# Kernel tuning notes

Hardware: AMD Instinct MI355X
Metric: run time of the kernel (lower is better)

The kernel has to match this reference:

```python
import jax, jax.numpy as jnp
import numpy as np

B, S, D, H = 4, 2048, 1024, 16
DK = D // H

def setup_inputs() -> dict:
    key = jax.random.key(0)
    ks = jax.random.split(key, 8)
    scale = 1.0 / np.sqrt(D)
    return {
        'q': jax.random.normal(ks[0], (B, S, D), jnp.float32),
        'k': jax.random.normal(ks[1], (B, S, D), jnp.float32),
        'v': jax.random.normal(ks[2], (B, S, D), jnp.float32),
        'Wq': jax.random.normal(ks[3], (D, D), jnp.float32) * scale,
        'bq': jnp.zeros((D,), jnp.float32),
        'Wk': jax.random.normal(ks[4], (D, D), jnp.float32) * scale,
        'bk': jnp.zeros((D,), jnp.float32),
        'Wv': jax.random.normal(ks[5], (D, D), jnp.float32) * scale,
        'bv': jnp.zeros((D,), jnp.float32),
        'Wo': jax.random.normal(ks[6], (D, D), jnp.float32) * scale,
        'bo': jnp.zeros((D,), jnp.float32),
    }

def reference(q, k, v, Wq, bq, Wk, bk, Wv, bv, Wo, bo):
    # Linear projections (torch Linear: x @ W.T + b; here W stored as [in,out])
    qp = q @ Wq + bq  # [B,S,D]
    kp = k @ Wk + bk
    vp = v @ Wv + bv
    # split heads -> [B,H,S,DK]
    qh = qp.reshape(B, S, H, DK).transpose(0, 2, 1, 3)
    kh = kp.reshape(B, S, H, DK).transpose(0, 2, 1, 3)
    vh = vp.reshape(B, S, H, DK).transpose(0, 2, 1, 3)
    scores = jnp.einsum('bhqd,bhkd->bhqk', qh, kh) / jnp.sqrt(jnp.float32(DK))
    attn = jax.nn.softmax(scores, axis=-1)  # [B,H,S,S]
    out = jnp.einsum('bhqk,bhkd->bhqd', attn, vh)
    out = out.transpose(0, 2, 1, 3).reshape(B, S, D)
    return out @ Wo + bo
```

## Files before the change

### kernel.cpp

```cpp
#include <hip/hip_runtime.h>
#include <math.h>

#define SEQ 2048
#define DIM 1024
#define NH 16

typedef short s8v __attribute__((ext_vector_type(8)));
typedef float f4v __attribute__((ext_vector_type(4)));

__device__ __forceinline__ unsigned short f2bf(float x) {
    unsigned u = __float_as_uint(x);
    u += 0x7FFFu + ((u >> 16) & 1u);
    return (unsigned short)(u >> 16);
}
__device__ __forceinline__ unsigned cvt_pk_bf16(float lo, float hi) {
    unsigned r;
    asm("v_cvt_pk_bf16_f32 %0, %1, %2" : "=v"(r) : "v"(lo), "v"(hi));
    return r;
}

__global__ void conv3_f32_bf16(const float* __restrict__ q, const float* __restrict__ k,
                               const float* __restrict__ v,
                               unsigned short* __restrict__ qb, unsigned short* __restrict__ kb,
                               unsigned short* __restrict__ vb, int n4) {
    const float* in = (blockIdx.y == 0) ? q : (blockIdx.y == 1) ? k : v;
    unsigned short* out = (blockIdx.y == 0) ? qb : (blockIdx.y == 1) ? kb : vb;
    int i = blockIdx.x * 256 + threadIdx.x;
    if (i >= n4) return;
    float4 x = ((const float4*)in)[i];
    ushort4 o;
    o.x = f2bf(x.x); o.y = f2bf(x.y); o.z = f2bf(x.z); o.w = f2bf(x.w);
    ((ushort4*)out)[i] = o;
}

__global__ __launch_bounds__(256)
void convT4_f32_bf16(const float* __restrict__ W0, const float* __restrict__ W1,
                     const float* __restrict__ W2, const float* __restrict__ W3,
                     unsigned short* __restrict__ T0, unsigned short* __restrict__ T1,
                     unsigned short* __restrict__ T2, unsigned short* __restrict__ T3) {
    const float* W = (blockIdx.z == 0) ? W0 : (blockIdx.z == 1) ? W1 : (blockIdx.z == 2) ? W2 : W3;
    unsigned short* WT = (blockIdx.z == 0) ? T0 : (blockIdx.z == 1) ? T1 : (blockIdx.z == 2) ? T2 : T3;
    __shared__ float T[64][65];
    const int t = threadIdx.x;
    const int n0 = blockIdx.x * 64, k0 = blockIdx.y * 64;
    #pragma unroll
    for (int i = 0; i < 4; i++) {
        int idx = t + i * 256;
        int r = idx >> 4, c4 = idx & 15;
        float4 v = *(const float4*)&W[(size_t)(k0 + r) * DIM + n0 + c4 * 4];
        T[r][c4 * 4 + 0] = v.x; T[r][c4 * 4 + 1] = v.y;
        T[r][c4 * 4 + 2] = v.z; T[r][c4 * 4 + 3] = v.w;
    }
    __syncthreads();
    #pragma unroll
    for (int i = 0; i < 4; i++) {
        int idx = t + i * 256;
        int rn = idx >> 4, c4 = idx & 15;
        ushort4 o;
        o.x = f2bf(T[c4 * 4 + 0][rn]);
        o.y = f2bf(T[c4 * 4 + 1][rn]);
        o.z = f2bf(T[c4 * 4 + 2][rn]);
        o.w = f2bf(T[c4 * 4 + 3][rn]);
        *(ushort4*)&WT[(size_t)(n0 + rn) * DIM + k0 + c4 * 4] = o;
    }
}

template<int MODE>
__device__ __forceinline__
void gemm_core(const unsigned short* __restrict__ A,
               const unsigned short* __restrict__ BT,
               const float* __restrict__ bias, void* __restrict__ outp,
               float scale, int bx, int by)
{
    __shared__ __align__(16) unsigned short As[128 * 64];
    __shared__ __align__(16) unsigned short Bs[128 * 64];
    const int t = threadIdx.x;
    const int lane = t & 63, w = t >> 6;
    const int l15 = lane & 15, quad = lane >> 4;
    const int bm = by * 128, bn = bx * 128;
    const int wm = (w & 1) * 64, wn = (w >> 1) * 64;
    const int lrow = lane >> 3, lcol = (lane & 7) * 8;

    f4v acc[4][4];
    #pragma unroll
    for (int mi = 0; mi < 4; mi++)
        #pragma unroll
        for (int ni = 0; ni < 4; ni++)
            acc[mi][ni] = (f4v){0.f, 0.f, 0.f, 0.f};

    for (int k0 = 0; k0 < DIM; k0 += 64) {
        __syncthreads();
        #pragma unroll
        for (int i = 0; i < 4; i++) {
            int ci = w + i * 4;
            int row = ci * 8 + lrow;
            __builtin_amdgcn_global_load_lds(
                (const __attribute__((address_space(1))) unsigned int*)
                    (A + (size_t)(bm + row) * DIM + k0 + lcol),
                (__attribute__((address_space(3))) unsigned int*)(As + ci * 8 * 64),
                16, 0, 0);
            __builtin_amdgcn_global_load_lds(
                (const __attribute__((address_space(1))) unsigned int*)
                    (BT + (size_t)(bn + row) * DIM + k0 + lcol),
                (__attribute__((address_space(3))) unsigned int*)(Bs + ci * 8 * 64),
                16, 0, 0);
        }
        __syncthreads();
        #pragma unroll
        for (int kc = 0; kc < 2; kc++) {
            const int ko = kc * 32 + quad * 8;
            s8v af[4], bf[4];
            #pragma unroll
            for (int mi = 0; mi < 4; mi++)
                af[mi] = *(const s8v*)&As[(wm + mi * 16 + l15) * 64 + ko];
            #pragma unroll
            for (int ni = 0; ni < 4; ni++)
                bf[ni] = *(const s8v*)&Bs[(wn + ni * 16 + l15) * 64 + ko];
            #pragma unroll
            for (int mi = 0; mi < 4; mi++)
                #pragma unroll
                for (int ni = 0; ni < 4; ni++)
                    acc[mi][ni] = __builtin_amdgcn_mfma_f32_16x16x32_bf16(
                        af[mi], bf[ni], acc[mi][ni], 0, 0, 0);
        }
    }

    #pragma unroll
    for (int mi = 0; mi < 4; mi++) {
        #pragma unroll
        for (int ni = 0; ni < 4; ni++) {
            #pragma unroll
            for (int r = 0; r < 4; r++) {
                int m = bm + wm + mi * 16 + quad * 4 + r;
                int n = bn + wn + ni * 16 + l15;
                float val = acc[mi][ni][r] + bias[n];
                if (MODE == 0) {
                    ((float*)outp)[(size_t)m * DIM + n] = val;
                } else {
                    val *= scale;
                    int b = m >> 11, s = m & (SEQ - 1);
                    int h = n >> 6, dk = n & 63;
                    ((unsigned short*)outp)[(((size_t)(b * NH + h)) * SEQ + s) * 64 + dk] = f2bf(val);
                }
            }
        }
    }
}

__global__ __launch_bounds__(256)
void qkv_gemm(const unsigned short* __restrict__ qb, const unsigned short* __restrict__ kb,
              const unsigned short* __restrict__ vb,
              const unsigned short* __restrict__ WqT, const unsigned short* __restrict__ WkT,
              const unsigned short* __restrict__ WvT,
              const float* __restrict__ bq, const float* __restrict__ bk,
              const float* __restrict__ bv,
              unsigned short* __restrict__ qp, unsigned short* __restrict__ kp,
              unsigned short* __restrict__ vp)
{
    const int z = blockIdx.z;
    const unsigned short* A  = (z == 0) ? qb : (z == 1) ? kb : vb;
    const unsigned short* BT = (z == 0) ? WqT : (z == 1) ? WkT : WvT;
    const float* bias        = (z == 0) ? bq : (z == 1) ? bk : bv;
    unsigned short* outp     = (z == 0) ? qp : (z == 1) ? kp : vp;
    float scale = (z == 0) ? 0.18033688011112042f : 1.0f;
    gemm_core<1>(A, BT, bias, outp, scale, blockIdx.x, blockIdx.y);
}

__global__ __launch_bounds__(256)
void out_gemm(const unsigned short* __restrict__ A, const unsigned short* __restrict__ BT,
              const float* __restrict__ bias, float* __restrict__ outp)
{
    gemm_core<0>(A, BT, bias, outp, 1.0f, blockIdx.x, blockIdx.y);
}

__global__ __launch_bounds__(256)
void transp_v(const unsigned short* __restrict__ vp, unsigned short* __restrict__ vpT) {
    __shared__ unsigned short T[64 * 72];
    const int t = threadIdx.x;
    const int bh = blockIdx.y, s0 = blockIdx.x * 64;
    const int r = t >> 3, c = (t & 7) * 8;
    #pragma unroll
    for (int i = 0; i < 2; i++) {
        int row = r + i * 32;
        *(s8v*)&T[row * 72 + c] = *(const s8v*)&vp[((size_t)bh * SEQ + s0 + row) * 64 + c];
    }
    __syncthreads();
    #pragma unroll
    for (int i = 0; i < 2; i++) {
        int d = r + i * 32;
        s8v o;
        #pragma unroll
        for (int j = 0; j < 8; j++) o[j] = (short)T[(c + j) * 72 + d];
        *(s8v*)&vpT[((size_t)bh * 64 + d) * SEQ + s0 + c] = o;
    }
}

__global__ __launch_bounds__(256)
void attn_mfma(const unsigned short* __restrict__ Q,
               const unsigned short* __restrict__ Kp,
               const unsigned short* __restrict__ VT,
               unsigned short* __restrict__ AO)
{
    __shared__ __align__(16) unsigned short Ks[64 * 72];
    __shared__ __align__(16) unsigned short Vs[64 * 72];
    __shared__ __align__(16) unsigned short Ps[4][32 * 72];
    const int t = threadIdx.x;
    const int lane = t & 63, w = t >> 6;
    const int l15 = lane & 15, quad = lane >> 4;
    const int bh = blockIdx.y, q0 = blockIdx.x * 128;

    const unsigned short* qbase = Q + ((size_t)bh * SEQ + q0 + w * 32) * 64;
    const unsigned short* kbase = Kp + (size_t)bh * SEQ * 64;
    const unsigned short* vtbase = VT + (size_t)bh * 64 * SEQ;

    s8v qf[2][2];
    #pragma unroll
    for (int qs = 0; qs < 2; qs++)
        #pragma unroll
        for (int kc = 0; kc < 2; kc++)
            qf[qs][kc] = *(const s8v*)&qbase[(qs * 16 + l15) * 64 + kc * 32 + quad * 8];

    f4v o_acc[2][4];
    #pragma unroll
    for (int qs = 0; qs < 2; qs++)
        #pragma unroll
        for (int df = 0; df < 4; df++) o_acc[qs][df] = (f4v){0.f, 0.f, 0.f, 0.f};
    float l_part[2] = {0.f, 0.f};

    const int srow = t >> 3, scol = (t & 7) * 8;
    unsigned short* Pw = (unsigned short*)Ps[w];

    s8v kreg[2], vreg[2];
    #pragma unroll
    for (int i = 0; i < 2; i++) {
        int row = srow + i * 32;
        kreg[i] = *(const s8v*)&kbase[(size_t)row * 64 + scol];
        vreg[i] = *(const s8v*)&vtbase[(size_t)row * SEQ + scol];
    }
    #pragma unroll
    for (int i = 0; i < 2; i++) {
        int row = srow + i * 32;
        *(s8v*)&Ks[row * 72 + scol] = kreg[i];
        *(s8v*)&Vs[row * 72 + scol] = vreg[i];
    }
    __syncthreads();

    for (int kt = 0; kt < 32; kt++) {
        if (kt < 31) {
            #pragma unroll
            for (int i = 0; i < 2; i++) {
                int row = srow + i * 32;
                kreg[i] = *(const s8v*)&kbase[((size_t)((kt + 1) * 64 + row)) * 64 + scol];
                vreg[i] = *(const s8v*)&vtbase[(size_t)row * SEQ + (kt + 1) * 64 + scol];
            }
        }

        f4v s_acc[2][4];
        #pragma unroll
        for (int qs = 0; qs < 2; qs++)
            #pragma unroll
            for (int mf = 0; mf < 4; mf++) s_acc[qs][mf] = (f4v){0.f, 0.f, 0.f, 0.f};
        __builtin_amdgcn_s_setprio(1);
        #pragma unroll
        for (int kc = 0; kc < 2; kc++) {
            const int ko = kc * 32 + quad * 8;
            #pragma unroll
            for (int mf = 0; mf < 4; mf++) {
                s8v kf = *(const s8v*)&Ks[(mf * 16 + l15) * 72 + ko];
                #pragma unroll
                for (int qs = 0; qs < 2; qs++)
                    s_acc[qs][mf] = __builtin_amdgcn_mfma_f32_16x16x32_bf16(
                        kf, qf[qs][kc], s_acc[qs][mf], 0, 0, 0);
            }
        }
        __builtin_amdgcn_s_setprio(0);

        #pragma unroll
        for (int qs = 0; qs < 2; qs++) {
            #pragma unroll
            for (int mf = 0; mf < 4; mf++) {
                float p0 = __builtin_amdgcn_exp2f(s_acc[qs][mf][0]);
                float p1 = __builtin_amdgcn_exp2f(s_acc[qs][mf][1]);
                float p2 = __builtin_amdgcn_exp2f(s_acc[qs][mf][2]);
                float p3 = __builtin_amdgcn_exp2f(s_acc[qs][mf][3]);
                l_part[qs] += (p0 + p1) + (p2 + p3);
                uint2 pk;
                pk.x = cvt_pk_bf16(p0, p1);
                pk.y = cvt_pk_bf16(p2, p3);
                *(uint2*)&Pw[(qs * 16 + l15) * 72 + mf * 16 + quad * 4] = pk;
            }
        }

        #pragma unroll
        for (int kc2 = 0; kc2 < 2; kc2++) {
            const int ko = kc2 * 32 + quad * 8;
            s8v pf0 = *(const s8v*)&Pw[(0 * 16 + l15) * 72 + ko];
            s8v pf1 = *(const s8v*)&Pw[(1 * 16 + l15) * 72 + ko];
            __builtin_amdgcn_s_setprio(1);
            #pragma unroll
            for (int df = 0; df < 4; df++) {
                s8v vf = *(const s8v*)&Vs[(df * 16 + l15) * 72 + ko];
                o_acc[0][df] = __builtin_amdgcn_mfma_f32_16x16x32_bf16(pf0, vf, o_acc[0][df], 0, 0, 0);
                o_acc[1][df] = __builtin_amdgcn_mfma_f32_16x16x32_bf16(pf1, vf, o_acc[1][df], 0, 0, 0);
            }
            __builtin_amdgcn_s_setprio(0);
        }

        __syncthreads();
        if (kt < 31) {
            #pragma unroll
            for (int i = 0; i < 2; i++) {
                int row = srow + i * 32;
                *(s8v*)&Ks[row * 72 + scol] = kreg[i];
                *(s8v*)&Vs[row * 72 + scol] = vreg[i];
            }
        }
        __syncthreads();
    }

    float lq[2][4];
    #pragma unroll
    for (int qs = 0; qs < 2; qs++) {
        float lt = l_part[qs];
        lt += __shfl_xor(lt, 16);
        lt += __shfl_xor(lt, 32);
        #pragma unroll
        for (int r = 0; r < 4; r++)
            lq[qs][r] = 1.0f / __shfl(lt, quad * 4 + r);
    }

    const int b = bh >> 4, h = bh & (NH - 1);
    #pragma unroll
    for (int qs = 0; qs < 2; qs++) {
        #pragma unroll
        for (int r = 0; r < 4; r++) {
            int s = q0 + w * 32 + qs * 16 + quad * 4 + r;
            #pragma unroll
            for (int df = 0; df < 4; df++)
                AO[((size_t)(b * SEQ + s)) * DIM + h * 64 + df * 16 + l15] =
                    f2bf(o_acc[qs][df][r] * lq[qs][r]);
        }
    }
}

extern "C" void kernel_launch(void* const* d_in, const int* in_sizes, int n_in,
                              void* d_out, int out_size, void* d_ws, size_t ws_size,
                              hipStream_t stream) {
    const float* q  = (const float*)d_in[0];
    const float* k  = (const float*)d_in[1];
    const float* v  = (const float*)d_in[2];
    const float* Wq = (const float*)d_in[3];
    const float* bq = (const float*)d_in[4];
    const float* Wk = (const float*)d_in[5];
    const float* bk = (const float*)d_in[6];
    const float* Wv = (const float*)d_in[7];
    const float* bv = (const float*)d_in[8];
    const float* Wo = (const float*)d_in[9];
    const float* bo = (const float*)d_in[10];
    float* out = (float*)d_out;

    const size_t MK = (size_t)4 * SEQ * DIM;
    const size_t WK = (size_t)DIM * DIM;
    unsigned short* wsu = (unsigned short*)d_ws;
    unsigned short* qb  = wsu;
    unsigned short* kb  = qb + MK;
    unsigned short* vb  = kb + MK;
    unsigned short* WqT = vb + MK;
    unsigned short* WkT = WqT + WK;
    unsigned short* WvT = WkT + WK;
    unsigned short* WoT = WvT + WK;
    unsigned short* qp  = WoT + WK;
    unsigned short* kp  = qp + MK;
    unsigned short* vp  = kp + MK;
    unsigned short* ao  = vp + MK;
    unsigned short* vpT = qb;

    const int n4 = (int)(MK / 4);
    conv3_f32_bf16<<<dim3((n4 + 255) / 256, 3), 256, 0, stream>>>(q, k, v, qb, kb, vb, n4);
    convT4_f32_bf16<<<dim3(16, 16, 4), 256, 0, stream>>>(Wq, Wk, Wv, Wo, WqT, WkT, WvT, WoT);

    qkv_gemm<<<dim3(DIM / 128, (4 * SEQ) / 128, 3), 256, 0, stream>>>(
        qb, kb, vb, WqT, WkT, WvT, bq, bk, bv, qp, kp, vp);

    transp_v<<<dim3(SEQ / 64, 4 * NH), 256, 0, stream>>>(vp, vpT);

    attn_mfma<<<dim3(SEQ / 128, 4 * NH), 256, 0, stream>>>(qp, kp, vpT, ao);

    out_gemm<<<dim3(DIM / 128, (4 * SEQ) / 128), 256, 0, stream>>>(ao, WoT, bo, out);
}
```

Measured before the change: 379.1 us.

## Fuse V transpose into QKV GEMM epilogue, MFMA row sums, polynomial exp2

The V projection GEMM now writes its output directly in the transposed [bh, d, s] layout through a new epilogue mode, so the separate transpose kernel and its extra memory pass are gone. The attention kernel computes the softmax denominator with an extra MFMA against a ones vector instead of scalar adds and cross-lane shuffles. It also replaces the hardware exp2 with a software polynomial plus ldexp. The polynomial costs more VALU instructions than the native exp2 and may slow the softmax stage. The transposed epilogue writes 4-element strided stores, which may coalesce less well than the old layout.

```diff
diff --git a/kernel.cpp b/kernel.cpp
--- a/kernel.cpp
+++ b/kernel.cpp
@@ -17,6 +17,16 @@
     unsigned r;
     asm("v_cvt_pk_bf16_f32 %0, %1, %2" : "=v"(r) : "v"(lo), "v"(hi));
     return r;
+}
+__device__ __forceinline__ float fast_exp2(float x) {
+    float r = __builtin_rintf(x);
+    float f = x - r;
+    int   e = (int)r;
+    float p = fmaf(f, 0.0096181291f, 0.0555041087f);
+    p = fmaf(f, p, 0.2402265069f);
+    p = fmaf(f, p, 0.6931471806f);
+    p = fmaf(f, p, 1.0f);
+    return ldexpf(p, e);
 }
 
 __global__ void conv3_f32_bf16(const float* __restrict__ q, const float* __restrict__ k,
@@ -129,18 +139,34 @@
     for (int mi = 0; mi < 4; mi++) {
         #pragma unroll
         for (int ni = 0; ni < 4; ni++) {
-            #pragma unroll
-            for (int r = 0; r < 4; r++) {
-                int m = bm + wm + mi * 16 + quad * 4 + r;
+            if (MODE == 2) {
+                ushort4 o;
+                #pragma unroll
+                for (int r = 0; r < 4; r++) {
+                    int m = bm + wm + mi * 16 + quad * 4 + r;
+                    int n = bn + wn + ni * 16 + l15;
+                    float val = acc[mi][ni][r] + bias[n];
+                    ((unsigned short*)&o)[r] = f2bf(val);
+                }
+                int m0 = bm + wm + mi * 16 + quad * 4;
                 int n = bn + wn + ni * 16 + l15;
-                float val = acc[mi][ni][r] + bias[n];
-                if (MODE == 0) {
-                    ((float*)outp)[(size_t)m * DIM + n] = val;
-                } else {
-                    val *= scale;
-                    int b = m >> 11, s = m & (SEQ - 1);
-                    int h = n >> 6, dk = n & 63;
-                    ((unsigned short*)outp)[(((size_t)(b * NH + h)) * SEQ + s) * 64 + dk] = f2bf(val);
+                int b = m0 >> 11, s = m0 & (SEQ - 1);
+                int h = n >> 6, dk = n & 63;
+                *(ushort4*)&((unsigned short*)outp)[(((size_t)(b * NH + h)) * 64 + dk) * SEQ + s] = o;
+            } else {
+                #pragma unroll
+                for (int r = 0; r < 4; r++) {
+                    int m = bm + wm + mi * 16 + quad * 4 + r;
+                    int n = bn + wn + ni * 16 + l15;
+                    float val = acc[mi][ni][r] + bias[n];
+                    if (MODE == 0) {
+                        ((float*)outp)[(size_t)m * DIM + n] = val;
+                    } else {
+                        val *= scale;
+                        int b = m >> 11, s = m & (SEQ - 1);
+                        int h = n >> 6, dk = n & 63;
+                        ((unsigned short*)outp)[(((size_t)(b * NH + h)) * SEQ + s) * 64 + dk] = f2bf(val);
+                    }
                 }
             }
         }
@@ -155,15 +181,16 @@
               const float* __restrict__ bq, const float* __restrict__ bk,
               const float* __restrict__ bv,
               unsigned short* __restrict__ qp, unsigned short* __restrict__ kp,
-              unsigned short* __restrict__ vp)
+              unsigned short* __restrict__ vpT)
 {
     const int z = blockIdx.z;
-    const unsigned short* A  = (z == 0) ? qb : (z == 1) ? kb : vb;
-    const unsigned short* BT = (z == 0) ? WqT : (z == 1) ? WkT : WvT;
-    const float* bias        = (z == 0) ? bq : (z == 1) ? bk : bv;
-    unsigned short* outp     = (z == 0) ? qp : (z == 1) ? kp : vp;
-    float scale = (z == 0) ? 0.18033688011112042f : 1.0f;
-    gemm_core<1>(A, BT, bias, outp, scale, blockIdx.x, blockIdx.y);
+    if (z == 0) {
+        gemm_core<1>(qb, WqT, bq, qp, 0.18033688011112042f, blockIdx.x, blockIdx.y);
+    } else if (z == 1) {
+        gemm_core<1>(kb, WkT, bk, kp, 1.0f, blockIdx.x, blockIdx.y);
+    } else {
+        gemm_core<2>(vb, WvT, bv, vpT, 1.0f, blockIdx.x, blockIdx.y);
+    }
 }
 
 __global__ __launch_bounds__(256)
@@ -171,28 +198,6 @@
               const float* __restrict__ bias, float* __restrict__ outp)
 {
     gemm_core<0>(A, BT, bias, outp, 1.0f, blockIdx.x, blockIdx.y);
-}
-
-__global__ __launch_bounds__(256)
-void transp_v(const unsigned short* __restrict__ vp, unsigned short* __restrict__ vpT) {
-    __shared__ unsigned short T[64 * 72];
-    const int t = threadIdx.x;
-    const int bh = blockIdx.y, s0 = blockIdx.x * 64;
-    const int r = t >> 3, c = (t & 7) * 8;
-    #pragma unroll
-    for (int i = 0; i < 2; i++) {
-        int row = r + i * 32;
-        *(s8v*)&T[row * 72 + c] = *(const s8v*)&vp[((size_t)bh * SEQ + s0 + row) * 64 + c];
-    }
-    __syncthreads();
-    #pragma unroll
-    for (int i = 0; i < 2; i++) {
-        int d = r + i * 32;
-        s8v o;
-        #pragma unroll
-        for (int j = 0; j < 8; j++) o[j] = (short)T[(c + j) * 72 + d];
-        *(s8v*)&vpT[((size_t)bh * 64 + d) * SEQ + s0 + c] = o;
-    }
 }
 
 __global__ __launch_bounds__(256)
@@ -225,7 +230,10 @@
     for (int qs = 0; qs < 2; qs++)
         #pragma unroll
         for (int df = 0; df < 4; df++) o_acc[qs][df] = (f4v){0.f, 0.f, 0.f, 0.f};
-    float l_part[2] = {0.f, 0.f};
+    f4v o_l[2];
+    o_l[0] = (f4v){0.f, 0.f, 0.f, 0.f};
+    o_l[1] = (f4v){0.f, 0.f, 0.f, 0.f};
+    const s8v ones = {0x3F80, 0x3F80, 0x3F80, 0x3F80, 0x3F80, 0x3F80, 0x3F80, 0x3F80};
 
     const int srow = t >> 3, scol = (t & 7) * 8;
     unsigned short* Pw = (unsigned short*)Ps[w];
@@ -279,11 +287,10 @@
         for (int qs = 0; qs < 2; qs++) {
             #pragma unroll
             for (int mf = 0; mf < 4; mf++) {
-                float p0 = __builtin_amdgcn_exp2f(s_acc[qs][mf][0]);
-                float p1 = __builtin_amdgcn_exp2f(s_acc[qs][mf][1]);
-                float p2 = __builtin_amdgcn_exp2f(s_acc[qs][mf][2]);
-                float p3 = __builtin_amdgcn_exp2f(s_acc[qs][mf][3]);
-                l_part[qs] += (p0 + p1) + (p2 + p3);
+                float p0 = fast_exp2(s_acc[qs][mf][0]);
+                float p1 = fast_exp2(s_acc[qs][mf][1]);
+                float p2 = fast_exp2(s_acc[qs][mf][2]);
+                float p3 = fast_exp2(s_acc[qs][mf][3]);
                 uint2 pk;
                 pk.x = cvt_pk_bf16(p0, p1);
                 pk.y = cvt_pk_bf16(p2, p3);
@@ -297,6 +304,8 @@
             s8v pf0 = *(const s8v*)&Pw[(0 * 16 + l15) * 72 + ko];
             s8v pf1 = *(const s8v*)&Pw[(1 * 16 + l15) * 72 + ko];
             __builtin_amdgcn_s_setprio(1);
+            o_l[0] = __builtin_amdgcn_mfma_f32_16x16x32_bf16(pf0, ones, o_l[0], 0, 0, 0);
+            o_l[1] = __builtin_amdgcn_mfma_f32_16x16x32_bf16(pf1, ones, o_l[1], 0, 0, 0);
             #pragma unroll
             for (int df = 0; df < 4; df++) {
                 s8v vf = *(const s8v*)&Vs[(df * 16 + l15) * 72 + ko];
@@ -318,27 +327,17 @@
         __syncthreads();
     }
 
-    float lq[2][4];
+    const int b = bh >> 4, h = bh & (NH - 1);
     #pragma unroll
     for (int qs = 0; qs < 2; qs++) {
-        float lt = l_part[qs];
-        lt += __shfl_xor(lt, 16);
-        lt += __shfl_xor(lt, 32);
-        #pragma unroll
-        for (int r = 0; r < 4; r++)
-            lq[qs][r] = 1.0f / __shfl(lt, quad * 4 + r);
-    }
-
-    const int b = bh >> 4, h = bh & (NH - 1);
-    #pragma unroll
-    for (int qs = 0; qs < 2; qs++) {
         #pragma unroll
         for (int r = 0; r < 4; r++) {
+            float lq = 1.0f / o_l[qs][r];
             int s = q0 + w * 32 + qs * 16 + quad * 4 + r;
             #pragma unroll
             for (int df = 0; df < 4; df++)
                 AO[((size_t)(b * SEQ + s)) * DIM + h * 64 + df * 16 + l15] =
-                    f2bf(o_acc[qs][df][r] * lq[qs][r]);
+                    f2bf(o_acc[qs][df][r] * lq);
         }
     }
 }
@@ -371,18 +370,15 @@
     unsigned short* WoT = WvT + WK;
     unsigned short* qp  = WoT + WK;
     unsigned short* kp  = qp + MK;
-    unsigned short* vp  = kp + MK;
-    unsigned short* ao  = vp + MK;
-    unsigned short* vpT = qb;
+    unsigned short* vpT = kp + MK;
+    unsigned short* ao  = vpT + MK;
 
     const int n4 = (int)(MK / 4);
     conv3_f32_bf16<<<dim3((n4 + 255) / 256, 3), 256, 0, stream>>>(q, k, v, qb, kb, vb, n4);
     convT4_f32_bf16<<<dim3(16, 16, 4), 256, 0, stream>>>(Wq, Wk, Wv, Wo, WqT, WkT, WvT, WoT);
 
     qkv_gemm<<<dim3(DIM / 128, (4 * SEQ) / 128, 3), 256, 0, stream>>>(
-        qb, kb, vb, WqT, WkT, WvT, bq, bk, bv, qp, kp, vp);
-
-    transp_v<<<dim3(SEQ / 64, 4 * NH), 256, 0, stream>>>(vp, vpT);
+        qb, kb, vb, WqT, WkT, WvT, bq, bk, bv, qp, kp, vpT);
 
     attn_mfma<<<dim3(SEQ / 128, 4 * NH), 256, 0, stream>>>(qp, kp, vpT, ao);
 
```

New measurement: 395.4 us. 4.3% more time.
